# Performance work log

Measured on AMD Instinct MI355X. Metric: run time of the kernel, lower is better.

The kernel has to match this reference:

```python
import jax, jax.numpy as jnp
import numpy as np

FS = 32000
HOP = 512
WIN_SIZES = [2048, 1024, 512, 256, 128, 64]
BAND_EDGES = [20.0, 80.0, 500.0, 1250.0, 2540.0, 4050.0, 15000.0]
ERB_STEP = 0.25
ERBS = np.arange(1.75, 39.0 + 1e-6, ERB_STEP)            # 150 ERB channels
FC = (10.0 ** (ERBS / 21.366) - 1.0) / 0.004368           # channel center freqs (Hz)
I0 = (2e-5) ** 2                                          # reference intensity (Pa^2)
LUT_X = np.linspace(0.0, 110.0, 88).astype(np.float32)    # LUT excitation grid (dB)
SIGMA = 0.08
P_INHIB = 1.5978
HALF = 8
_g = np.arange(-HALF, HALF + 1) * ERB_STEP
GAUSS = np.exp(-_g ** 2 / (2.0 * SIGMA ** 2))
GAUSS = (GAUSS / GAUSS.sum()).astype(np.float32)

def _components():
    # frequency-dependent window selection: longest window -> lowest band
    freqs, idxs = [], []
    for w, N in enumerate(WIN_SIZES):
        fb = np.arange(N // 2 + 1) * FS / N
        sel = np.where((fb >= BAND_EDGES[w]) & (fb < BAND_EDGES[w + 1]))[0]
        idxs.append(sel)
        freqs.append(fb[sel])
    return np.concatenate(freqs), idxs
COMP_FREQS, WIN_BIN_IDX = _components()  # K ~ 67 sparse components

def _roex():
    erbw = 24.673 * (0.004368 * FC + 1.0)
    p = 4.0 * FC / erbw
    g = np.abs(COMP_FREQS[:, None] / FC[None, :] - 1.0)
    return ((1.0 + p * g) * np.exp(-p * g)).astype(np.float32)
ROEX_W = _roex()  # (K, 150)

def _ear_filter(x, h):
    # Stage 1: outer/middle ear FIR, same-length output
    B, C, T = x.shape
    k = h[::-1].reshape(1, 1, -1)
    y = jax.lax.conv_general_dilated(x.reshape(B * C, 1, T), k, (1,),
                                     [(h.shape[0] // 2, h.shape[0] // 2)],
                                     dimension_numbers=("NCH", "OIH", "NCH"))
    return y.reshape(B, C, T)

def _sparse_spectrum(x):
    # Stage 2: multi-resolution FFT analysis -> linear intensities at sparse comps
    B, T = x.shape
    F = T // HOP
    pad = WIN_SIZES[0] // 2
    xp = jnp.pad(x, ((0, 0), (pad, pad)))
    centers = pad + jnp.arange(F) * HOP
    outs = []
    for N, bins in zip(WIN_SIZES, WIN_BIN_IDX):
        idx = (centers - N // 2)[:, None] + jnp.arange(N)   # (F, N)
        frames = xp[:, idx]                                 # (B, F, N)
        n = jnp.arange(N, dtype=x.dtype)
        win = 0.5 - 0.5 * jnp.cos(2.0 * jnp.pi * n / (N - 1))
        spec = jnp.fft.rfft(frames * win, axis=-1)
        amp = 2.0 * jnp.abs(spec[..., jnp.asarray(bins)]) / win.sum()
        outs.append(0.5 * amp ** 2)                          # tone intensity
    return jnp.concatenate(outs, axis=-1)                    # (B, F, K)

def _agc(x, a_att, a_rel):
    # asymmetric attack/release AGC over frame axis (axis=1)
    def step(s, xt):
        a = jnp.where(xt > s, a_att, a_rel)
        s = a * xt + (1.0 - a) * s
        return s, s
    xt = jnp.moveaxis(x, 1, 0)
    _, y = jax.lax.scan(step, jnp.zeros_like(xt[0]), xt)
    return jnp.moveaxis(y, 0, 1)

def _smooth(n):
    # Gaussian spatial smoothing along ERB-channel axis
    B, F, C = n.shape
    k = jnp.asarray(GAUSS[::-1].copy(), n.dtype).reshape(1, 1, -1)
    y = jax.lax.conv_general_dilated(n.reshape(B * F, 1, C), k, (1,),
                                     [(HALF, HALF)],
                                     dimension_numbers=("NCH", "OIH", "NCH"))
    return y.reshape(B, F, C)

def _forward(audio, ear_fir, lut_values):
    y = _ear_filter(audio, ear_fir)
    lut_x = jnp.asarray(LUT_X)
    W = jnp.asarray(ROEX_W, audio.dtype)
    stl = []
    for ch in range(2):
        I = _sparse_spectrum(y[:, ch])                       # (B, F, K)
        E = I @ W                                            # roex excitation (B, F, 150)
        E_db = 10.0 * jnp.log10(E / I0 + 1e-12)
        n_inst = jnp.interp(jnp.clip(E_db, lut_x[0], lut_x[-1]), lut_x, lut_values)
        stl.append(_agc(n_inst, 0.045, 0.033))               # short-term loudness
    sl, sr = _smooth(stl[0]), _smooth(stl[1])
    sech = lambda z: 1.0 / jnp.cosh(z)
    stl_l = (sl * sech(P_INHIB * sr)).sum(-1) / 4.0          # (B, F)
    stl_r = (sr * sech(P_INHIB * sl)).sum(-1) / 4.0
    ltl_l = _agc(stl_l[..., None], 0.01, 0.00133)[..., 0]
    ltl_r = _agc(stl_r[..., None], 0.01, 0.00133)[..., 0]
    sLoud = stl_l + stl_r
    lLoud = ltl_l + ltl_r
    mLoud = lLoud.max(axis=-1)
    return sLoud, lLoud, mLoud

def setup_inputs():
    key = jax.random.key(0)
    k1, k2, k3 = jax.random.split(key, 3)
    audio = jax.random.normal(k1, (16, 2, 320000), dtype=jnp.float32) * 0.05
    ear_fir = jax.random.normal(k2, (1025,), dtype=jnp.float32) * 0.03
    lut_values = jnp.sort(jax.random.uniform(k3, (88,), dtype=jnp.float32)) * 40.0
    return {"audio": audio, "ear_fir": ear_fir, "lut_values": lut_values}

def reference(audio, ear_fir, lut_values):
    return _forward(audio, ear_fir, lut_values)
```

## Files before the change

kernel.cpp:

```cpp
#include <hip/hip_runtime.h>
#include <hip/hip_bf16.h>
#include <math.h>

#define T_LEN   320000
#define NB      16
#define NROWS   32
#define NFRAMES 625
#define NCOMP   67
#define NCH     150
#define HOPSZ   512
#define BREP    8
#define BSZ     491520

typedef __attribute__((ext_vector_type(8))) _Float16 half8v;
typedef __attribute__((ext_vector_type(8))) short short8v;
typedef __attribute__((ext_vector_type(4))) float f32x4;

__constant__ int cW_N[6]  = {2048,1024,512,256,128,64};
__constant__ int cW_K0[6] = {2,3,8,10,11,9};
__constant__ int cW_CB[7] = {0,4,17,29,40,46,67};
__constant__ int cW_CO[7] = {0,8192,21504,27648,30464,31232,32576};
__constant__ int dNEp[6]  = {3072,2048,1536,1280,1152,1152};
__constant__ int dNEr[6]  = {3072,2048,1536,1280,1152,1088};
__constant__ int dBTb[7]  = {0,147456,245760,319488,380928,436224,491520};
__constant__ int dCPB[6]  = {12,8,6,5,5,5};
__constant__ int dCKB[7]  = {0,48,152,224,279,309,414};
__constant__ int eW[8] = {0,0,0,1,2,3,4,5};
__constant__ int eF[8] = {0,1,624,0,0,0,0,0};

__constant__ int tBb[12]   = {147456,180224,0,380928,0,436224,245760,454656,270336,473088,319488,339968};
__constant__ int tNEp[12]  = {2048,2048,3072,1152,3072,1152,1536,1152,1536,1152,1280,1280};
__constant__ int tStb[12]  = {512,512,0,960,0,992,768,992,768,992,896,896};
__constant__ int tKs0[12]  = {0,0,0,0,48,0,0,0,0,0,0,0};
__constant__ int tKs1[12]  = {64,64,48,36,96,36,48,36,48,36,40,40};
__constant__ int tJadd[12] = {4,12,0,40,0,46,17,54,25,62,29,37};
__constant__ int tNbL[12]  = {13,5,4,6,4,21,12,13,4,5,11,3};
__constant__ int tMode[12] = {0,0,1,0,2,0,0,0,0,0,0,0};
__constant__ int wStart[8] = {0,1,2,4,6,8,10,11};
__constant__ int wCnt[8]   = {1,1,2,2,2,2,1,1};

__device__ __forceinline__ unsigned short f2bf(float v) {
  unsigned u = __float_as_uint(v);
  return (unsigned short)((u + 0x7FFFu + ((u >> 16) & 1u)) >> 16);
}

__global__ __launch_bounds__(256) void setup_k(const float* __restrict__ h,
                                               const float* __restrict__ x,
                                               float2* __restrict__ coeff,
                                               float* __restrict__ Wmat,
                                               float* __restrict__ gauss,
                                               unsigned short* __restrict__ Bf,
                                               float* __restrict__ ye,
                                               unsigned short* __restrict__ Wb16) {
  __shared__ float sm[3585];
  const int bid = blockIdx.x, tid = threadIdx.x;
  if (bid < 167) {
    int gid = bid * 256 + tid;
    if (gid < 32576) {
      int w = 0;
      while (gid >= cW_CO[w + 1]) ++w;
      int local = gid - cW_CO[w];
      int N = cW_N[w];
      int jloc = local / N;
      int n = local - jloc * N;
      int k = cW_K0[w] + jloc;
      float win = 0.5f - 0.5f * cospif(2.0f * (float)n / (float)(N - 1));
      int r = (int)(((long long)k * (long long)n) % (long long)N);
      float ang = 2.0f * (float)r / (float)N;
      float scale = sqrtf(2.0f) / (0.5f * (float)(N - 1));
      float wc = win * scale;
      coeff[gid] = make_float2(wc * cospif(ang), wc * sinpif(ang));
    } else if (gid < 32576 + NCOMP * NCH) {
      int t = gid - 32576;
      int j = t / NCH, c = t - j * NCH;
      float erb = 1.75f + 0.25f * (float)c;
      float fc = (exp10f(erb * (1.0f / 21.366f)) - 1.0f) * (1.0f / 0.004368f);
      float erbw = 24.673f * (0.004368f * fc + 1.0f);
      float p = 4.0f * fc / erbw;
      int w = 0;
      while (j >= cW_CB[w + 1]) ++w;
      float freq = (float)(cW_K0[w] + (j - cW_CB[w])) * (32000.0f / (float)cW_N[w]);
      float g = fabsf(freq / fc - 1.0f);
      float pg = p * g;
      Wmat[j * NCH + c] = (1.0f + pg) * expf(-pg);
    } else if (gid == 32576 + NCOMP * NCH) {
      float tmp[17]; float s = 0.0f;
      for (int k = 0; k < 17; ++k) {
        float g = ((float)k - 8.0f) * 0.25f;
        tmp[k] = expf(-g * g / (2.0f * 0.08f * 0.08f));
        s += tmp[k];
      }
      for (int k = 0; k < 17; ++k) gauss[k] = tmp[k] / s;
    }
  } else if (bid < 581) {
    float* cre_l = sm;
    float* cim_l = sm + 1280;
    float* hs    = sm + 2560;
    const int b2 = bid - 167;
    int w = 0;
    while (b2 >= dCKB[w + 1]) ++w;
    const int local = b2 - dCKB[w];
    const int jloc = local / dCPB[w];
    const int chunk = local - jloc * dCPB[w];
    const int N = cW_N[w];
    const int k = cW_K0[w] + jloc;
    const int NEp = dNEp[w], NEr = dNEr[w];
    const int v0 = chunk * 256;
    const int nlo_blk = max(0, v0 - 1024);
    const int nhi_blk = min(N - 1, v0 + 255);
    const int cnt_n = nhi_blk - nlo_blk + 1;
    const float scale = sqrtf(2.0f) / (0.5f * (float)(N - 1));
    for (int i = tid; i < 1025; i += 256) hs[i] = h[i];
    for (int i = tid; i < cnt_n; i += 256) {
      int n = nlo_blk + i;
      float win = 0.5f - 0.5f * cospif(2.0f * (float)n / (float)(N - 1));
      int r = (int)(((long long)k * (long long)n) % (long long)N);
      float ang = 2.0f * (float)r / (float)N;
      float wc = win * scale;
      cre_l[i] = wc * cospif(ang);
      cim_l[i] = wc * sinpif(ang);
    }
    __syncthreads();
    const int v = v0 + tid;
    if (v >= NEp) return;
    float re = 0.0f, im = 0.0f;
    if (v < NEr) {
      const int n0 = max(nlo_blk, v - 1024);
      const int n1 = min(nhi_blk, v);
      float r0 = 0.f, r1 = 0.f, r2 = 0.f, r3 = 0.f;
      float m0 = 0.f, m1 = 0.f, m2 = 0.f, m3 = 0.f;
      int n = n0;
      const int hoff = 1024 - v, coff = -nlo_blk;
      for (; n + 3 <= n1; n += 4) {
        float h0 = hs[n + hoff],     h1 = hs[n + 1 + hoff];
        float h2 = hs[n + 2 + hoff], h3 = hs[n + 3 + hoff];
        r0 = fmaf(cre_l[n + coff],     h0, r0); m0 = fmaf(cim_l[n + coff],     h0, m0);
        r1 = fmaf(cre_l[n + 1 + coff], h1, r1); m1 = fmaf(cim_l[n + 1 + coff], h1, m1);
        r2 = fmaf(cre_l[n + 2 + coff], h2, r2); m2 = fmaf(cim_l[n + 2 + coff], h2, m2);
        r3 = fmaf(cre_l[n + 3 + coff], h3, r3); m3 = fmaf(cim_l[n + 3 + coff], h3, m3);
      }
      for (; n <= n1; ++n) {
        float hv = hs[n + hoff];
        r0 = fmaf(cre_l[n + coff], hv, r0);
        m0 = fmaf(cim_l[n + coff], hv, m0);
      }
      re = (r0 + r1) + (r2 + r3);
      im = (m0 + m1) + (m2 + m3);
    }
    size_t o0 = (size_t)dBTb[w] + (size_t)(2 * jloc) * NEp + v;
    size_t o1 = o0 + NEp;
    _Float16 hr = (_Float16)re;
    _Float16 hi2 = (_Float16)im;
    unsigned short hrb = *(unsigned short*)&hr;
    unsigned short hib = *(unsigned short*)&hi2;
#pragma unroll
    for (int cp = 0; cp < BREP; ++cp) {
      Bf[(size_t)cp * BSZ + o0] = hrb;
      Bf[(size_t)cp * BSZ + o1] = hib;
    }
  } else if (bid < 965) {
    float* xl = sm;
    float* hs = sm + 1280;
    const int b2 = bid - 581;
    const int chunk = b2 % 12, row = b2 / 12;
    const size_t rowoff = (size_t)row * T_LEN;
    const int i0 = chunk * 256;
    const int pos0 = (i0 < 1536) ? i0 : 318464 + (i0 - 1536);
    for (int i = tid; i < 1025; i += 256) hs[i] = h[i];
    for (int i = tid; i < 1280; i += 256) {
      int g = pos0 - 512 + i;
      xl[i] = ((unsigned)g < (unsigned)T_LEN) ? x[rowoff + g] : 0.0f;
    }
    __syncthreads();
    float a0 = 0.0f, a1 = 0.0f, a2 = 0.0f, a3 = 0.0f;
    const int d = tid + 1024;
    for (int m = 0; m < 1024; m += 4) {
      a0 = fmaf(hs[m],     xl[d - m],     a0);
      a1 = fmaf(hs[m + 1], xl[d - m - 1], a1);
      a2 = fmaf(hs[m + 2], xl[d - m - 2], a2);
      a3 = fmaf(hs[m + 3], xl[d - m - 3], a3);
    }
    float acc = ((a0 + a1) + (a2 + a3)) + hs[1024] * xl[d - 1024];
    ye[(size_t)row * 3072 + i0 + tid] = acc;
  } else {
    for (int u = tid; u < 160 * 96; u += 256) {
      int c = u / 96, j = u - (u / 96) * 96;
      float val = 0.0f;
      if (c < NCH && j < NCOMP) {
        float erb = 1.75f + 0.25f * (float)c;
        float fc = (exp10f(erb * (1.0f / 21.366f)) - 1.0f) * (1.0f / 0.004368f);
        float erbw = 24.673f * (0.004368f * fc + 1.0f);
        float p = 4.0f * fc / erbw;
        int w = 0;
        while (j >= cW_CB[w + 1]) ++w;
        float freq = (float)(cW_K0[w] + (j - cW_CB[w])) * (32000.0f / (float)cW_N[w]);
        float g = fabsf(freq / fc - 1.0f);
        float pg = p * g;
        val = (1.0f + pg) * expf(-pg);
      }
      Wb16[u] = f2bf(val);
    }
  }
}

#define TILE_X 18944
#define SWZ4(i) ((i) ^ ((((i) >> 9) & 15) << 3))

__global__ __launch_bounds__(512) void sparse2(const float* __restrict__ x,
                                               const unsigned short* __restrict__ Bf,
                                               const float2* __restrict__ coeff,
                                               const float* __restrict__ ye,
                                               float* __restrict__ Ibuf) {
  __shared__ __align__(16) unsigned short sxh[TILE_X];
  __shared__ float redA[512];
  const int b = blockIdx.x, tid = threadIdx.x;
  if (b < 640) {
    const int fblk = b % 20, row = b / 20;
    const int f0 = fblk * 32;
    const float* xr = x + (size_t)row * T_LEN;
    const unsigned short* Bc = Bf + (size_t)(b & (BREP - 1)) * BSZ;
    const int lo = f0 * HOPSZ - 1536;
    for (int i = 4 * tid; i < TILE_X; i += 2048) {
      const int g = lo + i;
      float v[4];
      if (g >= 0 && g + 4 <= T_LEN) {
        float4 p = *(const float4*)(xr + g);
        v[0] = p.x; v[1] = p.y; v[2] = p.z; v[3] = p.w;
      } else {
#pragma unroll
        for (int q = 0; q < 4; ++q) {
          int gg = g + q;
          v[q] = ((unsigned)gg < (unsigned)T_LEN) ? xr[gg] : 0.0f;
        }
      }
      unsigned short h4[4];
#pragma unroll
      for (int q = 0; q < 4; ++q) {
        _Float16 hv = (_Float16)v[q];
        h4[q] = *(unsigned short*)&hv;
      }
      const int is = SWZ4(i);
      *(ushort4*)(sxh + is) = make_ushort4(h4[0], h4[1], h4[2], h4[3]);
    }
    __syncthreads();
    const int wv = tid >> 6, lane = tid & 63;
    const int fidx = lane & 15, kg = lane >> 4;
    const int t0 = wStart[wv], tcnt = wCnt[wv];
    f32x4 pA = (f32x4){0.f,0.f,0.f,0.f};
    f32x4 pB = (f32x4){0.f,0.f,0.f,0.f};
    for (int ti = t0; ti < t0 + tcnt; ++ti) {
      const int NEp = tNEp[ti];
      const int ks0 = tKs0[ti], ks1 = tKs1[ti];
      const unsigned short* Bp = Bc + tBb[ti] + fidx * NEp + kg * 8;
      const int ibase = fidx * 512 + tStb[ti] + kg * 8;
      f32x4 acc0 = (f32x4){0.f,0.f,0.f,0.f};
      f32x4 acc1 = (f32x4){0.f,0.f,0.f,0.f};
#pragma unroll 2
      for (int kk = ks0; kk < ks1; ++kk) {
        const int ko = kk * 32;
        half8v bv = *(const half8v*)(Bp + ko);
        half8v a0 = *(const half8v*)(sxh + SWZ4(ibase + ko));
        half8v a1 = *(const half8v*)(sxh + SWZ4(ibase + 8192 + ko));
        acc0 = __builtin_amdgcn_mfma_f32_16x16x32_f16(a0, bv, acc0, 0, 0, 0);
        acc1 = __builtin_amdgcn_mfma_f32_16x16x32_f16(a1, bv, acc1, 0, 0, 0);
      }
      const int mode = tMode[ti];
      if (mode == 0) {
        const int jadd = tJadd[ti], nbl = tNbL[ti];
        const int fh = fidx >> 1;
        const bool jvalid = !(fidx & 1) && fh < nbl;
#pragma unroll
        for (int r = 0; r < 4; ++r) {
          float v0 = acc0[r];
          float sq0 = v0 * v0;
          sq0 += __shfl_xor(sq0, 1);
          int fA = f0 + kg * 4 + r;
          if (jvalid && fA != 0)
            Ibuf[((size_t)row * NFRAMES + fA) * NCOMP + jadd + fh] = sq0;
          float v1 = acc1[r];
          float sq1 = v1 * v1;
          sq1 += __shfl_xor(sq1, 1);
          int fB = f0 + 16 + kg * 4 + r;
          if (jvalid && fB < NFRAMES)
            Ibuf[((size_t)row * NFRAMES + fB) * NCOMP + jadd + fh] = sq1;
        }
      } else if (mode == 1) {
#pragma unroll
        for (int r = 0; r < 4; ++r) {
          redA[lane * 4 + r] = acc0[r];
          redA[256 + lane * 4 + r] = acc1[r];
        }
      } else {
        pA = acc0; pB = acc1;
      }
    }
    __syncthreads();
    if (wv == 3) {
#pragma unroll
      for (int r = 0; r < 4; ++r) {
        float v0 = pA[r] + redA[lane * 4 + r];
        float sq0 = v0 * v0;
        sq0 += __shfl_xor(sq0, 1);
        int fA = f0 + kg * 4 + r;
        float v1 = pB[r] + redA[256 + lane * 4 + r];
        float sq1 = v1 * v1;
        sq1 += __shfl_xor(sq1, 1);
        int fB = f0 + 16 + kg * 4 + r;
        if (!(fidx & 1)) {
          int j = fidx >> 1;
          if (j < 4) {
            bool eA = (fA == 0) || (fA == 1) || (fA == 624);
            if (!eA) Ibuf[((size_t)row * NFRAMES + fA) * NCOMP + j] = sq0;
            bool eB = (fB == 1) || (fB == 624);
            if (fB < NFRAMES && !eB) Ibuf[((size_t)row * NFRAMES + fB) * NCOMP + j] = sq1;
          }
        }
      }
    }
  } else {
    const int row = b - 640;
    float* yl = (float*)sxh;
    for (int i = tid; i < 3072; i += 512) yl[i] = ye[(size_t)row * 3072 + i];
    __syncthreads();
    const int wv = tid >> 6, lane = tid & 63;
    const int w = eW[wv], f = eF[wv];
    const int N = cW_N[w];
    const int nb = cW_CB[w + 1] - cW_CB[w];
    for (int jl = 0; jl < nb; ++jl) {
      const float2* cf = coeff + cW_CO[w] + (size_t)jl * N;
      float re = 0.0f, im = 0.0f;
      for (int n = lane; n < N; n += 64) {
        int pos = f * HOPSZ - (N >> 1) + n;
        if ((unsigned)pos < (unsigned)T_LEN) {
          int yi = (pos < 1536) ? pos : (pos - 318464 + 1536);
          float yv = yl[yi];
          float2 cs = cf[n];
          re = fmaf(yv, cs.x, re);
          im = fmaf(yv, cs.y, im);
        }
      }
#pragma unroll
      for (int off = 32; off > 0; off >>= 1) {
        re += __shfl_xor(re, off);
        im += __shfl_xor(im, off);
      }
      if (lane == 0)
        Ibuf[((size_t)row * NFRAMES + f) * NCOMP + (cW_CB[w] + jl)] = re * re + im * im;
    }
  }
}

__global__ __launch_bounds__(256) void espec(const float* __restrict__ Ibuf,
                                             const unsigned short* __restrict__ Wb16,
                                             const float* __restrict__ lut,
                                             float* __restrict__ ninst) {
  __shared__ __align__(16) unsigned short sxA[64 * 104];
  __shared__ float luts[88];
  const int row = blockIdx.y;
  const int fB = blockIdx.x * 64;
  const int tid = threadIdx.x;
  if (tid < 88) luts[tid] = lut[tid];
  for (int u = tid; u < 64 * 52; u += 256) ((unsigned*)sxA)[u] = 0;
  __syncthreads();
  for (int u = tid; u < 64 * NCOMP; u += 256) {
    int fl = u / NCOMP, j = u - fl * NCOMP;
    int f = fB + fl;
    float v = (f < NFRAMES) ? Ibuf[((size_t)row * NFRAMES + f) * NCOMP + j] : 0.0f;
    sxA[fl * 104 + j] = f2bf(v);
  }
  __syncthreads();
  const int wv = tid >> 6, lane = tid & 63;
  const int fidx = lane & 15, kg = lane >> 4;
  const unsigned short* Ap = sxA + (wv * 16 + fidx) * 104 + kg * 8;
  short8v a0 = *(const short8v*)(Ap);
  short8v a1 = *(const short8v*)(Ap + 32);
  short8v a2 = *(const short8v*)(Ap + 64);
  f32x4 acc[10];
#pragma unroll
  for (int ct = 0; ct < 10; ++ct) acc[ct] = (f32x4){0.f,0.f,0.f,0.f};
#pragma unroll
  for (int ct = 0; ct < 10; ++ct) {
    const unsigned short* Bp = Wb16 + (ct * 16 + fidx) * 96 + kg * 8;
    short8v b0 = *(const short8v*)(Bp);
    short8v b1 = *(const short8v*)(Bp + 32);
    short8v b2 = *(const short8v*)(Bp + 64);
    acc[ct] = __builtin_amdgcn_mfma_f32_16x16x32_bf16(a0, b0, acc[ct], 0, 0, 0);
    acc[ct] = __builtin_amdgcn_mfma_f32_16x16x32_bf16(a1, b1, acc[ct], 0, 0, 0);
    acc[ct] = __builtin_amdgcn_mfma_f32_16x16x32_bf16(a2, b2, acc[ct], 0, 0, 0);
  }
  const int fbase = fB + wv * 16 + kg * 4;
#pragma unroll
  for (int ct = 0; ct < 10; ++ct) {
    const int c = ct * 16 + fidx;
    if (c < NCH) {
#pragma unroll
      for (int r = 0; r < 4; ++r) {
        const int f = fbase + r;
        if (f < NFRAMES) {
          float e = acc[ct][r];
          float edb = 3.0102999566f * __log2f(fmaf(e, 2.5e9f, 1e-12f));
          float xv = fminf(fmaxf(edb, 0.0f), 110.0f);
          float u2 = xv * (87.0f / 110.0f);
          int i0 = (int)u2; if (i0 > 86) i0 = 86;
          float fr = u2 - (float)i0;
          ninst[((size_t)row * NFRAMES + f) * NCH + c] =
              fmaf(luts[i0 + 1] - luts[i0], fr, luts[i0]);
        }
      }
    }
  }
}

__global__ __launch_bounds__(64) void agc1(const float* __restrict__ ninst,
                                           float* __restrict__ stl) {
  int idx = blockIdx.x * 64 + threadIdx.x;
  if (idx >= NROWS * NCH) return;
  int row = idx / NCH, c = idx - row * NCH;
  const float* src = ninst + (size_t)row * NFRAMES * NCH + c;
  float* dst = stl + (size_t)row * NFRAMES * NCH + c;
  float buf[16], cur[16];
#pragma unroll
  for (int i = 0; i < 16; ++i) buf[i] = src[(size_t)i * NCH];
  float s = 0.0f;
  for (int fb = 0; fb < 608; fb += 16) {
#pragma unroll
    for (int i = 0; i < 16; ++i) cur[i] = buf[i];
#pragma unroll
    for (int i = 0; i < 16; ++i) buf[i] = src[(size_t)(fb + 16 + i) * NCH];
#pragma unroll
    for (int j = 0; j < 16; ++j) {
      float xv = cur[j];
      float a = (xv > s) ? 0.045f : 0.033f;
      s = a * xv + (1.0f - a) * s;
      dst[(size_t)(fb + j) * NCH] = s;
    }
  }
#pragma unroll
  for (int j = 0; j < 16; ++j) {
    float xv = buf[j];
    float a = (xv > s) ? 0.045f : 0.033f;
    s = a * xv + (1.0f - a) * s;
    dst[(size_t)(608 + j) * NCH] = s;
  }
  float xv = src[(size_t)624 * NCH];
  float a = (xv > s) ? 0.045f : 0.033f;
  s = a * xv + (1.0f - a) * s;
  dst[(size_t)624 * NCH] = s;
}

__global__ __launch_bounds__(256) void combine(const float* __restrict__ stl,
                                               const float* __restrict__ gauss,
                                               float* __restrict__ outL,
                                               float* __restrict__ outR) {
  __shared__ float sl[8][168], sr[8][168], gsh[17];
  const int b = blockIdx.y, fb = blockIdx.x * 8;
  const int tid = threadIdx.x;
  if (tid < 17) gsh[tid] = gauss[tid];
  for (int u = tid; u < 8 * 168; u += 256) {
    int fi = u / 168, c = u - fi * 168;
    sl[fi][c] = 0.0f; sr[fi][c] = 0.0f;
  }
  __syncthreads();
  for (int u = tid; u < 8 * 300; u += 256) {
    int fi = u / 300, r = u - fi * 300;
    int f = fb + fi;
    if (f < NFRAMES) {
      int ch = (r < NCH) ? 0 : 1;
      int c = (r < NCH) ? r : r - NCH;
      float v = stl[((size_t)(b * 2 + ch) * NFRAMES + f) * NCH + c];
      if (ch == 0) sl[fi][8 + c] = v; else sr[fi][8 + c] = v;
    }
  }
  __syncthreads();
  const int wv = tid >> 6, lane = tid & 63;
#pragma unroll
  for (int fi2 = 0; fi2 < 2; ++fi2) {
    const int fi = wv * 2 + fi2;
    const int f = fb + fi;
    float pvl = 0.0f, pvr = 0.0f;
#pragma unroll
    for (int s = 0; s < 3; ++s) {
      int c = lane + 64 * s;
      if (c < NCH) {
        float smL = 0.0f, smR = 0.0f;
#pragma unroll
        for (int t = 0; t < 17; ++t) {
          smL = fmaf(gsh[t], sl[fi][c + t], smL);
          smR = fmaf(gsh[t], sr[fi][c + t], smR);
        }
        float tR = __expf(-1.5978f * smR);
        float tL = __expf(-1.5978f * smL);
        pvl += smL * (2.0f * tR / fmaf(tR, tR, 1.0f));
        pvr += smR * (2.0f * tL / fmaf(tL, tL, 1.0f));
      }
    }
#pragma unroll
    for (int off = 32; off > 0; off >>= 1) {
      pvl += __shfl_xor(pvl, off);
      pvr += __shfl_xor(pvr, off);
    }
    if (lane == 0 && f < NFRAMES) {
      outL[b * NFRAMES + f] = pvl * 0.25f;
      outR[b * NFRAMES + f] = pvr * 0.25f;
    }
  }
}

__global__ __launch_bounds__(256) void final_k(const float* __restrict__ sLst,
                                               const float* __restrict__ sRst,
                                               float* __restrict__ out) {
  __shared__ float Ls[NB][641];
  __shared__ float Rs[NB][641];
  __shared__ float Lv[NB][641];
  const int tid = threadIdx.x;
  for (int u = tid; u < NB * NFRAMES; u += 256) {
    int b = u / NFRAMES, f = u - b * NFRAMES;
    float a = sLst[u];
    float c = sRst[u];
    Ls[b][f] = a;
    Rs[b][f] = c;
    out[u] = a + c;
  }
  __syncthreads();
  if (tid < NB) {
    const int b = tid;
    float ll = 0.0f, lr = 0.0f, mx = -3.4e38f;
    for (int f = 0; f < NFRAMES; ++f) {
      float a = Ls[b][f];
      float c = Rs[b][f];
      float aa = (a > ll) ? 0.01f : 0.00133f;
      ll = aa * a + (1.0f - aa) * ll;
      float ab = (c > lr) ? 0.01f : 0.00133f;
      lr = ab * c + (1.0f - ab) * lr;
      float lv = ll + lr;
      Lv[b][f] = lv;
      mx = fmaxf(mx, lv);
    }
    out[2 * NB * NFRAMES + b] = mx;
  }
  __syncthreads();
  for (int u = tid; u < NB * NFRAMES; u += 256) {
    int b = u / NFRAMES, f = u - b * NFRAMES;
    out[NB * NFRAMES + u] = Lv[b][f];
  }
}

extern "C" void kernel_launch(void* const* d_in, const int* in_sizes, int n_in,
                              void* d_out, int out_size, void* d_ws, size_t ws_size,
                              hipStream_t stream) {
  const float* audio = (const float*)d_in[0];
  const float* ear   = (const float*)d_in[1];
  const float* lut   = (const float*)d_in[2];
  char* ws = (char*)d_ws;

  unsigned short* BfT    = (unsigned short*)(ws);
  float2*         coeffO = (float2*)(ws + 7864320);
  float*          Wmat   = (float*)(ws + 8124928);
  float*          gauss  = (float*)(ws + 8165128);
  float*          yedge  = (float*)(ws + 8165376);
  float*          Ibuf   = (float*)(ws + 8558592);
  float*          ninst  = (float*)(ws + 13918592);
  float*          stl    = (float*)(ws + 25918592);
  float*          stlL   = (float*)(ws + 37918592);
  float*          stlR   = (float*)(ws + 37958592);
  unsigned short* Wb16   = (unsigned short*)(ws + 37998592);

  hipLaunchKernelGGL(setup_k, dim3(966), dim3(256), 0, stream,
                     ear, audio, coeffO, Wmat, gauss, BfT, yedge, Wb16);
  hipLaunchKernelGGL(sparse2, dim3(672), dim3(512), 0, stream,
                     audio, BfT, coeffO, yedge, Ibuf);
  hipLaunchKernelGGL(espec, dim3(10, 32), dim3(256), 0, stream, Ibuf, Wb16, lut, ninst);
  hipLaunchKernelGGL(agc1, dim3(75), dim3(64), 0, stream, ninst, stl);
  hipLaunchKernelGGL(combine, dim3(79, 16), dim3(256), 0, stream, stl, gauss, stlL, stlR);
  hipLaunchKernelGGL(final_k, dim3(1), dim3(256), 0, stream, stlL, stlR, (float*)d_out);
}
```

Measured before the change: 184.4 us.

## Vectorize FIR tap loads, add nontemporal hints, deepen AGC prefetch

Loads the FIR taps from shared memory as float4 in the edge-convolution path and aligns the shared buffer to make that legal. Switches the audio reads in the sparse-spectrum kernel and the intermediate intensity buffer stores and loads to nontemporal builtins to reduce cache pollution. Doubles the register prefetch depth in the serial AGC scan from 16 to 32 frames to hide more global-load latency. The deeper prefetch raises register pressure, and the nontemporal hints may hurt if Ibuf would otherwise be served from cache by the next kernel.

New measurement: 188.1 us. Within noise of the previous version (+2.0%).

```diff
diff --git a/kernel.cpp b/kernel.cpp
--- a/kernel.cpp
+++ b/kernel.cpp
@@ -52,7 +52,7 @@
                                                unsigned short* __restrict__ Bf,
                                                float* __restrict__ ye,
                                                unsigned short* __restrict__ Wb16) {
-  __shared__ float sm[3585];
+  __shared__ __align__(16) float sm[3585];
   const int bid = blockIdx.x, tid = threadIdx.x;
   if (bid < 167) {
     int gid = bid * 256 + tid;
@@ -174,11 +174,13 @@
     __syncthreads();
     float a0 = 0.0f, a1 = 0.0f, a2 = 0.0f, a3 = 0.0f;
     const int d = tid + 1024;
+    const float4* hs4 = (const float4*)hs;
     for (int m = 0; m < 1024; m += 4) {
-      a0 = fmaf(hs[m],     xl[d - m],     a0);
-      a1 = fmaf(hs[m + 1], xl[d - m - 1], a1);
-      a2 = fmaf(hs[m + 2], xl[d - m - 2], a2);
-      a3 = fmaf(hs[m + 3], xl[d - m - 3], a3);
+      float4 hv = hs4[m >> 2];
+      a0 = fmaf(hv.x, xl[d - m],     a0);
+      a1 = fmaf(hv.y, xl[d - m - 1], a1);
+      a2 = fmaf(hv.z, xl[d - m - 2], a2);
+      a3 = fmaf(hv.w, xl[d - m - 3], a3);
     }
     float acc = ((a0 + a1) + (a2 + a3)) + hs[1024] * xl[d - 1024];
     ye[(size_t)row * 3072 + i0 + tid] = acc;
@@ -224,13 +226,13 @@
       const int g = lo + i;
       float v[4];
       if (g >= 0 && g + 4 <= T_LEN) {
-        float4 p = *(const float4*)(xr + g);
-        v[0] = p.x; v[1] = p.y; v[2] = p.z; v[3] = p.w;
+        f32x4 p = __builtin_nontemporal_load((const f32x4*)(xr + g));
+        v[0] = p[0]; v[1] = p[1]; v[2] = p[2]; v[3] = p[3];
       } else {
 #pragma unroll
         for (int q = 0; q < 4; ++q) {
           int gg = g + q;
-          v[q] = ((unsigned)gg < (unsigned)T_LEN) ? xr[gg] : 0.0f;
+          v[q] = ((unsigned)gg < (unsigned)T_LEN) ? __builtin_nontemporal_load(xr + gg) : 0.0f;
         }
       }
       unsigned short h4[4];
@@ -276,13 +278,13 @@
           sq0 += __shfl_xor(sq0, 1);
           int fA = f0 + kg * 4 + r;
           if (jvalid && fA != 0)
-            Ibuf[((size_t)row * NFRAMES + fA) * NCOMP + jadd + fh] = sq0;
+            __builtin_nontemporal_store(sq0, &Ibuf[((size_t)row * NFRAMES + fA) * NCOMP + jadd + fh]);
           float v1 = acc1[r];
           float sq1 = v1 * v1;
           sq1 += __shfl_xor(sq1, 1);
           int fB = f0 + 16 + kg * 4 + r;
           if (jvalid && fB < NFRAMES)
-            Ibuf[((size_t)row * NFRAMES + fB) * NCOMP + jadd + fh] = sq1;
+            __builtin_nontemporal_store(sq1, &Ibuf[((size_t)row * NFRAMES + fB) * NCOMP + jadd + fh]);
         }
       } else if (mode == 1) {
 #pragma unroll
@@ -310,9 +312,9 @@
           int j = fidx >> 1;
           if (j < 4) {
             bool eA = (fA == 0) || (fA == 1) || (fA == 624);
-            if (!eA) Ibuf[((size_t)row * NFRAMES + fA) * NCOMP + j] = sq0;
+            if (!eA) __builtin_nontemporal_store(sq0, &Ibuf[((size_t)row * NFRAMES + fA) * NCOMP + j]);
             bool eB = (fB == 1) || (fB == 624);
-            if (fB < NFRAMES && !eB) Ibuf[((size_t)row * NFRAMES + fB) * NCOMP + j] = sq1;
+            if (fB < NFRAMES && !eB) __builtin_nontemporal_store(sq1, &Ibuf[((size_t)row * NFRAMES + fB) * NCOMP + j]);
           }
         }
       }
@@ -365,7 +367,7 @@
   for (int u = tid; u < 64 * NCOMP; u += 256) {
     int fl = u / NCOMP, j = u - fl * NCOMP;
     int f = fB + fl;
-    float v = (f < NFRAMES) ? Ibuf[((size_t)row * NFRAMES + f) * NCOMP + j] : 0.0f;
+    float v = (f < NFRAMES) ? __builtin_nontemporal_load(&Ibuf[((size_t)row * NFRAMES + f) * NCOMP + j]) : 0.0f;
     sxA[fl * 104 + j] = f2bf(v);
   }
   __syncthreads();
@@ -418,17 +420,17 @@
   int row = idx / NCH, c = idx - row * NCH;
   const float* src = ninst + (size_t)row * NFRAMES * NCH + c;
   float* dst = stl + (size_t)row * NFRAMES * NCH + c;
-  float buf[16], cur[16];
-#pragma unroll
-  for (int i = 0; i < 16; ++i) buf[i] = src[(size_t)i * NCH];
+  float buf[32], cur[32];
+#pragma unroll
+  for (int i = 0; i < 32; ++i) buf[i] = src[(size_t)i * NCH];
   float s = 0.0f;
-  for (int fb = 0; fb < 608; fb += 16) {
-#pragma unroll
-    for (int i = 0; i < 16; ++i) cur[i] = buf[i];
-#pragma unroll
-    for (int i = 0; i < 16; ++i) buf[i] = src[(size_t)(fb + 16 + i) * NCH];
-#pragma unroll
-    for (int j = 0; j < 16; ++j) {
+  for (int fb = 0; fb < 576; fb += 32) {
+#pragma unroll
+    for (int i = 0; i < 32; ++i) cur[i] = buf[i];
+#pragma unroll
+    for (int i = 0; i < 32; ++i) buf[i] = src[(size_t)(fb + 32 + i) * NCH];
+#pragma unroll
+    for (int j = 0; j < 32; ++j) {
       float xv = cur[j];
       float a = (xv > s) ? 0.045f : 0.033f;
       s = a * xv + (1.0f - a) * s;
@@ -436,16 +438,18 @@
     }
   }
 #pragma unroll
-  for (int j = 0; j < 16; ++j) {
+  for (int j = 0; j < 32; ++j) {
     float xv = buf[j];
     float a = (xv > s) ? 0.045f : 0.033f;
     s = a * xv + (1.0f - a) * s;
-    dst[(size_t)(608 + j) * NCH] = s;
-  }
-  float xv = src[(size_t)624 * NCH];
-  float a = (xv > s) ? 0.045f : 0.033f;
-  s = a * xv + (1.0f - a) * s;
-  dst[(size_t)624 * NCH] = s;
+    dst[(size_t)(576 + j) * NCH] = s;
+  }
+  for (int f = 608; f < 625; ++f) {
+    float xv = src[(size_t)f * NCH];
+    float a = (xv > s) ? 0.045f : 0.033f;
+    s = a * xv + (1.0f - a) * s;
+    dst[(size_t)f * NCH] = s;
+  }
 }
 
 __global__ __launch_bounds__(256) void combine(const float* __restrict__ stl,
```
